# Performance work log

Hardware: AMD Instinct MI355X
Metric: run time of the kernel (lower is better)

The kernel has to match this reference:

```python
import jax, jax.numpy as jnp
import numpy as np


def setup_inputs() -> dict:
    key = jax.random.key(0)
    ks = jax.random.split(key, 5)
    B, S, D, H, E = 2, 2048, 1024, 2816, 8
    x = jax.random.normal(ks[0], (B, S, D), dtype=jnp.float32)
    Wg = jax.random.normal(ks[1], (E, D), dtype=jnp.float32) * 0.02
    W1 = jax.random.normal(ks[2], (E, H, D), dtype=jnp.float32) * 0.02
    W2 = jax.random.normal(ks[3], (E, H, D), dtype=jnp.float32) * 0.02
    W3 = jax.random.normal(ks[4], (E, D, H), dtype=jnp.float32) * 0.02
    return {"x": x, "Wg": Wg, "W1": W1, "W2": W2, "W3": W3}


TOP_K = 2


def reference(x, Wg, W1, W2, W3):
    B, S, D = x.shape
    E = Wg.shape[0]
    xt = x.reshape(B * S, D)  # [T, D]
    # gating: raw logits, NO softmax (matches original module)
    scores = xt @ Wg.T  # [T, E]
    topk_scores, topk_idx = jax.lax.top_k(scores, TOP_K)  # [T, K]
    # dense per-expert SwiGLU FFN over all tokens, combined with sparse weights
    gate = jax.nn.silu(jnp.einsum('td,ehd->teh', xt, W1))  # [T, E, H]
    up = jnp.einsum('td,ehd->teh', xt, W2)                 # [T, E, H]
    y = jnp.einsum('teh,edh->ted', gate * up, W3)           # [T, E, D]
    # combine weights: w[t, e] = sum_k topk_scores[t, k] * (topk_idx[t, k] == e)
    onehot = jax.nn.one_hot(topk_idx, E, dtype=x.dtype)     # [T, K, E]
    w = jnp.einsum('tke,tk->te', onehot, topk_scores)       # [T, E]
    out = jnp.einsum('te,ted->td', w, y)                    # [T, D]
    return out.reshape(B, S, D)
```

## Files before the change

kernel.cpp:

```cpp
#include <hip/hip_runtime.h>
#include <hip/hip_bf16.h>


#define T_TOK 4096
#define DDIM 1024
#define HDIM 2816
#define NEXP 8

typedef __attribute__((ext_vector_type(8))) short short8;
typedef __attribute__((ext_vector_type(4))) short short4v;
typedef __attribute__((ext_vector_type(4))) float floatx4;

__device__ __forceinline__ short f2bf(float f) {
  union { float f; unsigned int u; } v; v.f = f;
  unsigned int u = v.u;
  u += 0x7FFFu + ((u >> 16) & 1u);
  return (short)(u >> 16);
}

__global__ __launch_bounds__(256) void zero_kernel(float4* __restrict__ out4, int* __restrict__ counts) {
  int i = blockIdx.x * 256 + threadIdx.x;
  out4[i] = make_float4(0.f, 0.f, 0.f, 0.f);
  if (blockIdx.x == 0 && threadIdx.x < NEXP) counts[threadIdx.x] = 0;
}

__global__ __launch_bounds__(64) void gating_kernel(const float* __restrict__ x,
    const float* __restrict__ Wg, short* __restrict__ xbf,
    int* __restrict__ counts, int* __restrict__ tlist, float* __restrict__ wlist) {
  int t = blockIdx.x;
  int lane = threadIdx.x;
  const float* xt = x + (size_t)t * DDIM;
  float xr[16];
#pragma unroll
  for (int j = 0; j < 16; ++j) xr[j] = xt[j * 64 + lane];
  short* xbt = xbf + (size_t)t * DDIM;
#pragma unroll
  for (int j = 0; j < 16; ++j) xbt[j * 64 + lane] = f2bf(xr[j]);
  float s[NEXP];
#pragma unroll
  for (int e = 0; e < NEXP; ++e) {
    const float* wge = Wg + e * DDIM;
    float p = 0.f;
#pragma unroll
    for (int j = 0; j < 16; ++j) p += xr[j] * wge[j * 64 + lane];
#pragma unroll
    for (int o = 32; o > 0; o >>= 1) p += __shfl_xor(p, o, 64);
    s[e] = p;
  }
  if (lane == 0) {
    int e1 = 0; float s1 = s[0];
#pragma unroll
    for (int e = 1; e < NEXP; ++e) if (s[e] > s1) { s1 = s[e]; e1 = e; }
    int e2 = -1; float s2 = -1e30f;
#pragma unroll
    for (int e = 0; e < NEXP; ++e) if (e != e1 && s[e] > s2) { s2 = s[e]; e2 = e; }
    int slot = atomicAdd(&counts[e1], 1);
    tlist[e1 * T_TOK + slot] = t; wlist[e1 * T_TOK + slot] = s1;
    slot = atomicAdd(&counts[e2], 1);
    tlist[e2 * T_TOK + slot] = t; wlist[e2 * T_TOK + slot] = s2;
  }
}

__global__ void offsets_kernel(const int* __restrict__ counts, int* __restrict__ offs) {
  if (threadIdx.x == 0 && blockIdx.x == 0) {
    int run = 0;
    for (int e = 0; e < NEXP; ++e) { offs[e] = run; run += counts[e]; }
  }
}

__global__ __launch_bounds__(256) void ffn1_kernel(const short* __restrict__ xbf,
    const float* __restrict__ W1, const float* __restrict__ W2,
    const int* __restrict__ counts, const int* __restrict__ offs,
    const int* __restrict__ tlist, short* __restrict__ hmat) {
  int e = blockIdx.z;
  int cnt = counts[e];
  int m0 = blockIdx.y * 128;
  if (m0 >= cnt) return;
  int n0 = blockIdx.x * 64;
  __shared__ __attribute__((aligned(16))) short As[128 * 40];
  __shared__ __attribute__((aligned(16))) short Bs1[64 * 40];
  __shared__ __attribute__((aligned(16))) short Bs2[64 * 40];
  __shared__ int toks[128];
  int tid = threadIdx.x;
  if (tid < 128) {
    int m = m0 + tid;
    toks[tid] = tlist[e * T_TOK + (m < cnt ? m : cnt - 1)];
  }
  __syncthreads();
  const float* W1e = W1 + (size_t)e * HDIM * DDIM + (size_t)n0 * DDIM;
  const float* W2e = W2 + (size_t)e * HDIM * DDIM + (size_t)n0 * DDIM;
  int lane = tid & 63, wid = tid >> 6;
  int wr = wid >> 1, wc = wid & 1;
  int lrow = lane & 15, lq = lane >> 4;
  floatx4 accg[4][2], accu[4][2];
#pragma unroll
  for (int i = 0; i < 4; ++i)
#pragma unroll
    for (int j = 0; j < 2; ++j) {
      accg[i][j] = (floatx4){0.f, 0.f, 0.f, 0.f};
      accu[i][j] = (floatx4){0.f, 0.f, 0.f, 0.f};
    }
  int ar0 = tid >> 2, ac0 = (tid & 3) * 8;
  int br0 = tid >> 3, bc0 = (tid & 7) * 4;
  int tokA0 = toks[ar0], tokA1 = toks[ar0 + 64];
  const short* xA0 = xbf + (size_t)tokA0 * DDIM + ac0;
  const short* xA1 = xbf + (size_t)tokA1 * DDIM + ac0;
  const float* pB1a = W1e + (size_t)br0 * DDIM + bc0;
  const float* pB1b = W1e + (size_t)(br0 + 32) * DDIM + bc0;
  const float* pB2a = W2e + (size_t)br0 * DDIM + bc0;
  const float* pB2b = W2e + (size_t)(br0 + 32) * DDIM + bc0;

  for (int kk = 0; kk < DDIM; kk += 32) {
    *(short8*)&As[ar0 * 40 + ac0]        = *(const short8*)(xA0 + kk);
    *(short8*)&As[(ar0 + 64) * 40 + ac0] = *(const short8*)(xA1 + kk);
    {
      float4 v1a = *(const float4*)(pB1a + kk);
      float4 v1b = *(const float4*)(pB1b + kk);
      float4 v2a = *(const float4*)(pB2a + kk);
      float4 v2b = *(const float4*)(pB2b + kk);
      *(short4v*)&Bs1[br0 * 40 + bc0]        = (short4v){f2bf(v1a.x), f2bf(v1a.y), f2bf(v1a.z), f2bf(v1a.w)};
      *(short4v*)&Bs1[(br0 + 32) * 40 + bc0] = (short4v){f2bf(v1b.x), f2bf(v1b.y), f2bf(v1b.z), f2bf(v1b.w)};
      *(short4v*)&Bs2[br0 * 40 + bc0]        = (short4v){f2bf(v2a.x), f2bf(v2a.y), f2bf(v2a.z), f2bf(v2a.w)};
      *(short4v*)&Bs2[(br0 + 32) * 40 + bc0] = (short4v){f2bf(v2b.x), f2bf(v2b.y), f2bf(v2b.z), f2bf(v2b.w)};
    }
    __syncthreads();
    short8 a[4], b1[2], b2[2];
#pragma unroll
    for (int mf = 0; mf < 4; ++mf)
      a[mf] = *(short8*)&As[(wr * 64 + mf * 16 + lrow) * 40 + lq * 8];
#pragma unroll
    for (int nf = 0; nf < 2; ++nf) {
      b1[nf] = *(short8*)&Bs1[(wc * 32 + nf * 16 + lrow) * 40 + lq * 8];
      b2[nf] = *(short8*)&Bs2[(wc * 32 + nf * 16 + lrow) * 40 + lq * 8];
    }
#pragma unroll
    for (int mf = 0; mf < 4; ++mf)
#pragma unroll
      for (int nf = 0; nf < 2; ++nf) {
        accg[mf][nf] = __builtin_amdgcn_mfma_f32_16x16x32_bf16(a[mf], b1[nf], accg[mf][nf], 0, 0, 0);
        accu[mf][nf] = __builtin_amdgcn_mfma_f32_16x16x32_bf16(a[mf], b2[nf], accu[mf][nf], 0, 0, 0);
      }
    __syncthreads();
  }
  int base = offs[e];
#pragma unroll
  for (int mf = 0; mf < 4; ++mf)
#pragma unroll
    for (int r = 0; r < 4; ++r) {
      int mloc = wr * 64 + mf * 16 + lq * 4 + r;
      if (m0 + mloc < cnt) {
        size_t row = (size_t)(base + m0 + mloc);
#pragma unroll
        for (int nf = 0; nf < 2; ++nf) {
          float g = accg[mf][nf][r];
          float u = accu[mf][nf][r];
          float h = g / (1.f + __expf(-g)) * u;
          hmat[row * HDIM + n0 + wc * 32 + nf * 16 + lrow] = f2bf(h);
        }
      }
    }
}

__global__ __launch_bounds__(256) void ffn2_kernel(const short* __restrict__ hmat,
    const float* __restrict__ W3,
    const int* __restrict__ counts, const int* __restrict__ offs,
    const int* __restrict__ tlist, const float* __restrict__ wlist,
    float* __restrict__ out) {
  int e = blockIdx.z;
  int cnt = counts[e];
  int m0 = blockIdx.y * 128;
  if (m0 >= cnt) return;
  int n0 = blockIdx.x * 128;
  __shared__ __attribute__((aligned(16))) short As[128 * 40];
  __shared__ __attribute__((aligned(16))) short Bs[128 * 40];
  __shared__ int toks[128];
  __shared__ float wts[128];
  int tid = threadIdx.x;
  if (tid < 128) {
    int m = m0 + tid;
    int mc = m < cnt ? m : cnt - 1;
    toks[tid] = tlist[e * T_TOK + mc];
    wts[tid] = (m < cnt) ? wlist[e * T_TOK + m] : 0.f;
  }
  __syncthreads();
  int base = offs[e];
  const float* W3e = W3 + (size_t)e * DDIM * HDIM + (size_t)n0 * HDIM;
  int lane = tid & 63, wid = tid >> 6;
  int wr = wid >> 1, wc = wid & 1;
  int lrow = lane & 15, lq = lane >> 4;
  floatx4 acc[4][4];
#pragma unroll
  for (int i = 0; i < 4; ++i)
#pragma unroll
    for (int j = 0; j < 4; ++j) acc[i][j] = (floatx4){0.f, 0.f, 0.f, 0.f};
  int ar0 = tid >> 2, ac0 = (tid & 3) * 8;
  int br0 = tid >> 3, bc0 = (tid & 7) * 4;
  int mA0 = m0 + ar0;       mA0 = mA0 < cnt ? mA0 : cnt - 1;
  int mA1 = m0 + ar0 + 64;  mA1 = mA1 < cnt ? mA1 : cnt - 1;
  const short* hA0 = hmat + (size_t)(base + mA0) * HDIM + ac0;
  const short* hA1 = hmat + (size_t)(base + mA1) * HDIM + ac0;

  for (int kk = 0; kk < HDIM; kk += 32) {
    *(short8*)&As[ar0 * 40 + ac0]        = *(const short8*)(hA0 + kk);
    *(short8*)&As[(ar0 + 64) * 40 + ac0] = *(const short8*)(hA1 + kk);
#pragma unroll
    for (int l = 0; l < 4; ++l) {
      int r = br0 + l * 32;
      float4 v = *(const float4*)(W3e + (size_t)r * HDIM + kk + bc0);
      *(short4v*)&Bs[r * 40 + bc0] = (short4v){f2bf(v.x), f2bf(v.y), f2bf(v.z), f2bf(v.w)};
    }
    __syncthreads();
    short8 a[4], b[4];
#pragma unroll
    for (int mf = 0; mf < 4; ++mf)
      a[mf] = *(short8*)&As[(wr * 64 + mf * 16 + lrow) * 40 + lq * 8];
#pragma unroll
    for (int nf = 0; nf < 4; ++nf)
      b[nf] = *(short8*)&Bs[(wc * 64 + nf * 16 + lrow) * 40 + lq * 8];
#pragma unroll
    for (int mf = 0; mf < 4; ++mf)
#pragma unroll
      for (int nf = 0; nf < 4; ++nf)
        acc[mf][nf] = __builtin_amdgcn_mfma_f32_16x16x32_bf16(a[mf], b[nf], acc[mf][nf], 0, 0, 0);
    __syncthreads();
  }
#pragma unroll
  for (int mf = 0; mf < 4; ++mf)
#pragma unroll
    for (int r = 0; r < 4; ++r) {
      int mloc = wr * 64 + mf * 16 + lq * 4 + r;
      if (m0 + mloc < cnt) {
        int t = toks[mloc];
        float w = wts[mloc];
        float* orow = out + (size_t)t * DDIM + n0 + wc * 64 + lrow;
#pragma unroll
        for (int nf = 0; nf < 4; ++nf)
          atomicAdd(orow + nf * 16, w * acc[mf][nf][r]);
      }
    }
}

extern "C" void kernel_launch(void* const* d_in, const int* in_sizes, int n_in,
                              void* d_out, int out_size, void* d_ws, size_t ws_size,
                              hipStream_t stream) {
  const float* x  = (const float*)d_in[0];
  const float* Wg = (const float*)d_in[1];
  const float* W1 = (const float*)d_in[2];
  const float* W2 = (const float*)d_in[3];
  const float* W3 = (const float*)d_in[4];
  float* out = (float*)d_out;
  char* ws = (char*)d_ws;
  int*   counts = (int*)(ws + 0);
  int*   offs   = (int*)(ws + 256);
  int*   tlist  = (int*)(ws + 512);
  float* wlist  = (float*)(ws + 512 + 131072);
  short* xbf    = (short*)(ws + 512 + 2 * 131072);
  short* hmat   = (short*)(ws + 8651264);

  zero_kernel<<<4096, 256, 0, stream>>>((float4*)out, counts);
  gating_kernel<<<4096, 64, 0, stream>>>(x, Wg, xbf, counts, tlist, wlist);
  offsets_kernel<<<1, 64, 0, stream>>>(counts, offs);
  ffn1_kernel<<<dim3(HDIM / 64, T_TOK / 128, NEXP), 256, 0, stream>>>(xbf, W1, W2, counts, offs, tlist, hmat);
  ffn2_kernel<<<dim3(DDIM / 128, T_TOK / 128, NEXP), 256, 0, stream>>>(hmat, W3, counts, offs, tlist, wlist, out);
}
```

Baseline: 653.6 us.

## Pre-convert weights to bf16, use direct global-to-LDS loads, split-K FFN2 with combine

Measured after the change: 622.2 us. -4.8%, faster.

```diff
diff --git a/kernel.cpp b/kernel.cpp
--- a/kernel.cpp
+++ b/kernel.cpp
@@ -1,5 +1,6 @@
 #include <hip/hip_runtime.h>
 #include <hip/hip_bf16.h>
+#include <stdint.h>
 
 
 #define T_TOK 4096
@@ -18,15 +19,39 @@
   return (short)(u >> 16);
 }
 
-__global__ __launch_bounds__(256) void zero_kernel(float4* __restrict__ out4, int* __restrict__ counts) {
-  int i = blockIdx.x * 256 + threadIdx.x;
-  out4[i] = make_float4(0.f, 0.f, 0.f, 0.f);
-  if (blockIdx.x == 0 && threadIdx.x < NEXP) counts[threadIdx.x] = 0;
-}
-
-__global__ __launch_bounds__(64) void gating_kernel(const float* __restrict__ x,
+__device__ __forceinline__ void gl2lds16(const void* g, void* l) {
+  __builtin_amdgcn_global_load_lds(
+      (const __attribute__((address_space(1))) void*)g,
+      (__attribute__((address_space(3))) void*)l, 16, 0, 0);
+}
+
+__global__ void offsets_kernel(const int* __restrict__ counts, int* __restrict__ offs) {
+  if (threadIdx.x == 0 && blockIdx.x == 0) {
+    int run = 0;
+    for (int e = 0; e < NEXP; ++e) { offs[e] = run; run += counts[e]; }
+  }
+}
+
+#define CONV_ELEM4 5767168
+__global__ __launch_bounds__(256) void convert_kernel(
+    const float* __restrict__ W1, const float* __restrict__ W2, const float* __restrict__ W3,
+    short* __restrict__ W1bf, short* __restrict__ W2bf, short* __restrict__ W3bf,
+    int* __restrict__ counts) {
+  if (blockIdx.x == 0 && blockIdx.y == 0 && threadIdx.x < NEXP) counts[threadIdx.x] = 0;
+  int z = blockIdx.y;
+  const float4* src = (const float4*)((z == 0) ? W1 : (z == 1) ? W2 : W3);
+  short4v* dst = (short4v*)((z == 0) ? W1bf : (z == 1) ? W2bf : W3bf);
+  size_t stride = (size_t)gridDim.x * 256;
+  for (size_t i = (size_t)blockIdx.x * 256 + threadIdx.x; i < CONV_ELEM4; i += stride) {
+    float4 v = src[i];
+    dst[i] = (short4v){f2bf(v.x), f2bf(v.y), f2bf(v.z), f2bf(v.w)};
+  }
+}
+
+__global__ __launch_bounds__(64) void gating_fast_kernel(const float* __restrict__ x,
     const float* __restrict__ Wg, short* __restrict__ xbf,
-    int* __restrict__ counts, int* __restrict__ tlist, float* __restrict__ wlist) {
+    int* __restrict__ counts, int* __restrict__ tlist,
+    int* __restrict__ re, int* __restrict__ rs, float* __restrict__ rw) {
   int t = blockIdx.x;
   int lane = threadIdx.x;
   const float* xt = x + (size_t)t * DDIM;
@@ -55,21 +80,16 @@
 #pragma unroll
     for (int e = 0; e < NEXP; ++e) if (e != e1 && s[e] > s2) { s2 = s[e]; e2 = e; }
     int slot = atomicAdd(&counts[e1], 1);
-    tlist[e1 * T_TOK + slot] = t; wlist[e1 * T_TOK + slot] = s1;
+    tlist[e1 * T_TOK + slot] = t;
+    re[2 * t] = e1; rs[2 * t] = slot; rw[2 * t] = s1;
     slot = atomicAdd(&counts[e2], 1);
-    tlist[e2 * T_TOK + slot] = t; wlist[e2 * T_TOK + slot] = s2;
-  }
-}
-
-__global__ void offsets_kernel(const int* __restrict__ counts, int* __restrict__ offs) {
-  if (threadIdx.x == 0 && blockIdx.x == 0) {
-    int run = 0;
-    for (int e = 0; e < NEXP; ++e) { offs[e] = run; run += counts[e]; }
-  }
-}
-
-__global__ __launch_bounds__(256) void ffn1_kernel(const short* __restrict__ xbf,
-    const float* __restrict__ W1, const float* __restrict__ W2,
+    tlist[e2 * T_TOK + slot] = t;
+    re[2 * t + 1] = e2; rs[2 * t + 1] = slot; rw[2 * t + 1] = s2;
+  }
+}
+
+__global__ __launch_bounds__(256) void ffn1_fast_kernel(const short* __restrict__ xbf,
+    const short* __restrict__ W1bf, const short* __restrict__ W2bf,
     const int* __restrict__ counts, const int* __restrict__ offs,
     const int* __restrict__ tlist, short* __restrict__ hmat) {
   int e = blockIdx.z;
@@ -77,9 +97,9 @@
   int m0 = blockIdx.y * 128;
   if (m0 >= cnt) return;
   int n0 = blockIdx.x * 64;
-  __shared__ __attribute__((aligned(16))) short As[128 * 40];
-  __shared__ __attribute__((aligned(16))) short Bs1[64 * 40];
-  __shared__ __attribute__((aligned(16))) short Bs2[64 * 40];
+  __shared__ __attribute__((aligned(16))) short As[128 * 32];
+  __shared__ __attribute__((aligned(16))) short Bs1[64 * 32];
+  __shared__ __attribute__((aligned(16))) short Bs2[64 * 32];
   __shared__ int toks[128];
   int tid = threadIdx.x;
   if (tid < 128) {
@@ -87,11 +107,21 @@
     toks[tid] = tlist[e * T_TOK + (m < cnt ? m : cnt - 1)];
   }
   __syncthreads();
-  const float* W1e = W1 + (size_t)e * HDIM * DDIM + (size_t)n0 * DDIM;
-  const float* W2e = W2 + (size_t)e * HDIM * DDIM + (size_t)n0 * DDIM;
-  int lane = tid & 63, wid = tid >> 6;
-  int wr = wid >> 1, wc = wid & 1;
+  int lane = tid & 63, w = tid >> 6;
+  int wr = w >> 1, wc = w & 1;
   int lrow = lane & 15, lq = lane >> 4;
+  int lr = lane >> 2;
+  int lc = (lane & 3) * 8;
+  const short* pA0 = xbf + (size_t)toks[w * 32 + lr] * DDIM + lc;
+  const short* pA1 = xbf + (size_t)toks[w * 32 + 16 + lr] * DDIM + lc;
+  const short* b1e = W1bf + (size_t)e * HDIM * DDIM;
+  const short* b2e = W2bf + (size_t)e * HDIM * DDIM;
+  const short* pB1 = b1e + (size_t)(n0 + w * 16 + lr) * DDIM + lc;
+  const short* pB2 = b2e + (size_t)(n0 + w * 16 + lr) * DDIM + lc;
+  void* lA0 = (void*)&As[(2 * w) * 512];
+  void* lA1 = (void*)&As[(2 * w + 1) * 512];
+  void* lB1 = (void*)&Bs1[w * 512];
+  void* lB2 = (void*)&Bs2[w * 512];
   floatx4 accg[4][2], accu[4][2];
 #pragma unroll
   for (int i = 0; i < 4; ++i)
@@ -100,38 +130,21 @@
       accg[i][j] = (floatx4){0.f, 0.f, 0.f, 0.f};
       accu[i][j] = (floatx4){0.f, 0.f, 0.f, 0.f};
     }
-  int ar0 = tid >> 2, ac0 = (tid & 3) * 8;
-  int br0 = tid >> 3, bc0 = (tid & 7) * 4;
-  int tokA0 = toks[ar0], tokA1 = toks[ar0 + 64];
-  const short* xA0 = xbf + (size_t)tokA0 * DDIM + ac0;
-  const short* xA1 = xbf + (size_t)tokA1 * DDIM + ac0;
-  const float* pB1a = W1e + (size_t)br0 * DDIM + bc0;
-  const float* pB1b = W1e + (size_t)(br0 + 32) * DDIM + bc0;
-  const float* pB2a = W2e + (size_t)br0 * DDIM + bc0;
-  const float* pB2b = W2e + (size_t)(br0 + 32) * DDIM + bc0;
-
   for (int kk = 0; kk < DDIM; kk += 32) {
-    *(short8*)&As[ar0 * 40 + ac0]        = *(const short8*)(xA0 + kk);
-    *(short8*)&As[(ar0 + 64) * 40 + ac0] = *(const short8*)(xA1 + kk);
-    {
-      float4 v1a = *(const float4*)(pB1a + kk);
-      float4 v1b = *(const float4*)(pB1b + kk);
-      float4 v2a = *(const float4*)(pB2a + kk);
-      float4 v2b = *(const float4*)(pB2b + kk);
-      *(short4v*)&Bs1[br0 * 40 + bc0]        = (short4v){f2bf(v1a.x), f2bf(v1a.y), f2bf(v1a.z), f2bf(v1a.w)};
-      *(short4v*)&Bs1[(br0 + 32) * 40 + bc0] = (short4v){f2bf(v1b.x), f2bf(v1b.y), f2bf(v1b.z), f2bf(v1b.w)};
-      *(short4v*)&Bs2[br0 * 40 + bc0]        = (short4v){f2bf(v2a.x), f2bf(v2a.y), f2bf(v2a.z), f2bf(v2a.w)};
-      *(short4v*)&Bs2[(br0 + 32) * 40 + bc0] = (short4v){f2bf(v2b.x), f2bf(v2b.y), f2bf(v2b.z), f2bf(v2b.w)};
-    }
+    gl2lds16(pA0, lA0);
+    gl2lds16(pA1, lA1);
+    gl2lds16(pB1, lB1);
+    gl2lds16(pB2, lB2);
+    pA0 += 32; pA1 += 32; pB1 += 32; pB2 += 32;
     __syncthreads();
     short8 a[4], b1[2], b2[2];
 #pragma unroll
     for (int mf = 0; mf < 4; ++mf)
-      a[mf] = *(short8*)&As[(wr * 64 + mf * 16 + lrow) * 40 + lq * 8];
+      a[mf] = *(short8*)&As[(wr * 64 + mf * 16 + lrow) * 32 + lq * 8];
 #pragma unroll
     for (int nf = 0; nf < 2; ++nf) {
-      b1[nf] = *(short8*)&Bs1[(wc * 32 + nf * 16 + lrow) * 40 + lq * 8];
-      b2[nf] = *(short8*)&Bs2[(wc * 32 + nf * 16 + lrow) * 40 + lq * 8];
+      b1[nf] = *(short8*)&Bs1[(wc * 32 + nf * 16 + lrow) * 32 + lq * 8];
+      b2[nf] = *(short8*)&Bs2[(wc * 32 + nf * 16 + lrow) * 32 + lq * 8];
     }
 #pragma unroll
     for (int mf = 0; mf < 4; ++mf)
@@ -161,62 +174,59 @@
     }
 }
 
-__global__ __launch_bounds__(256) void ffn2_kernel(const short* __restrict__ hmat,
-    const float* __restrict__ W3,
+#define KSPLIT 2
+#define KHALF (HDIM / KSPLIT)
+__global__ __launch_bounds__(256) void ffn2_fast_kernel(const short* __restrict__ hmat,
+    const short* __restrict__ W3bf,
     const int* __restrict__ counts, const int* __restrict__ offs,
-    const int* __restrict__ tlist, const float* __restrict__ wlist,
-    float* __restrict__ out) {
+    float* __restrict__ ypart0, float* __restrict__ ypart1) {
   int e = blockIdx.z;
   int cnt = counts[e];
   int m0 = blockIdx.y * 128;
   if (m0 >= cnt) return;
-  int n0 = blockIdx.x * 128;
-  __shared__ __attribute__((aligned(16))) short As[128 * 40];
-  __shared__ __attribute__((aligned(16))) short Bs[128 * 40];
-  __shared__ int toks[128];
-  __shared__ float wts[128];
+  int ks = blockIdx.x >> 3;
+  int n0 = (blockIdx.x & 7) * 128;
+  int k0 = ks * KHALF;
+  float* ypart = ks ? ypart1 : ypart0;
+  int base = offs[e];
+  __shared__ __attribute__((aligned(16))) short As[128 * 32];
+  __shared__ __attribute__((aligned(16))) short Bs[128 * 32];
   int tid = threadIdx.x;
-  if (tid < 128) {
-    int m = m0 + tid;
-    int mc = m < cnt ? m : cnt - 1;
-    toks[tid] = tlist[e * T_TOK + mc];
-    wts[tid] = (m < cnt) ? wlist[e * T_TOK + m] : 0.f;
-  }
-  __syncthreads();
-  int base = offs[e];
-  const float* W3e = W3 + (size_t)e * DDIM * HDIM + (size_t)n0 * HDIM;
-  int lane = tid & 63, wid = tid >> 6;
-  int wr = wid >> 1, wc = wid & 1;
+  int lane = tid & 63, w = tid >> 6;
+  int wr = w >> 1, wc = w & 1;
   int lrow = lane & 15, lq = lane >> 4;
+  int lr = lane >> 2;
+  int lc = (lane & 3) * 8;
+  int gA0 = m0 + w * 32 + lr;      gA0 = gA0 < cnt ? gA0 : cnt - 1;
+  int gA1 = m0 + w * 32 + 16 + lr; gA1 = gA1 < cnt ? gA1 : cnt - 1;
+  const short* pA0 = hmat + (size_t)(base + gA0) * HDIM + k0 + lc;
+  const short* pA1 = hmat + (size_t)(base + gA1) * HDIM + k0 + lc;
+  const short* W3e = W3bf + (size_t)e * DDIM * HDIM;
+  const short* pB0 = W3e + (size_t)(n0 + w * 32 + lr) * HDIM + k0 + lc;
+  const short* pB1 = W3e + (size_t)(n0 + w * 32 + 16 + lr) * HDIM + k0 + lc;
+  void* lA0 = (void*)&As[(2 * w) * 512];
+  void* lA1 = (void*)&As[(2 * w + 1) * 512];
+  void* lB0 = (void*)&Bs[(2 * w) * 512];
+  void* lB1 = (void*)&Bs[(2 * w + 1) * 512];
   floatx4 acc[4][4];
 #pragma unroll
   for (int i = 0; i < 4; ++i)
 #pragma unroll
     for (int j = 0; j < 4; ++j) acc[i][j] = (floatx4){0.f, 0.f, 0.f, 0.f};
-  int ar0 = tid >> 2, ac0 = (tid & 3) * 8;
-  int br0 = tid >> 3, bc0 = (tid & 7) * 4;
-  int mA0 = m0 + ar0;       mA0 = mA0 < cnt ? mA0 : cnt - 1;
-  int mA1 = m0 + ar0 + 64;  mA1 = mA1 < cnt ? mA1 : cnt - 1;
-  const short* hA0 = hmat + (size_t)(base + mA0) * HDIM + ac0;
-  const short* hA1 = hmat + (size_t)(base + mA1) * HDIM + ac0;
-
-  for (int kk = 0; kk < HDIM; kk += 32) {
-    *(short8*)&As[ar0 * 40 + ac0]        = *(const short8*)(hA0 + kk);
-    *(short8*)&As[(ar0 + 64) * 40 + ac0] = *(const short8*)(hA1 + kk);
-#pragma unroll
-    for (int l = 0; l < 4; ++l) {
-      int r = br0 + l * 32;
-      float4 v = *(const float4*)(W3e + (size_t)r * HDIM + kk + bc0);
-      *(short4v*)&Bs[r * 40 + bc0] = (short4v){f2bf(v.x), f2bf(v.y), f2bf(v.z), f2bf(v.w)};
-    }
+  for (int kk = 0; kk < KHALF; kk += 32) {
+    gl2lds16(pA0, lA0);
+    gl2lds16(pA1, lA1);
+    gl2lds16(pB0, lB0);
+    gl2lds16(pB1, lB1);
+    pA0 += 32; pA1 += 32; pB0 += 32; pB1 += 32;
     __syncthreads();
     short8 a[4], b[4];
 #pragma unroll
     for (int mf = 0; mf < 4; ++mf)
-      a[mf] = *(short8*)&As[(wr * 64 + mf * 16 + lrow) * 40 + lq * 8];
+      a[mf] = *(short8*)&As[(wr * 64 + mf * 16 + lrow) * 32 + lq * 8];
 #pragma unroll
     for (int nf = 0; nf < 4; ++nf)
-      b[nf] = *(short8*)&Bs[(wc * 64 + nf * 16 + lrow) * 40 + lq * 8];
+      b[nf] = *(short8*)&Bs[(wc * 64 + nf * 16 + lrow) * 32 + lq * 8];
 #pragma unroll
     for (int mf = 0; mf < 4; ++mf)
 #pragma unroll
@@ -230,14 +240,30 @@
     for (int r = 0; r < 4; ++r) {
       int mloc = wr * 64 + mf * 16 + lq * 4 + r;
       if (m0 + mloc < cnt) {
-        int t = toks[mloc];
-        float w = wts[mloc];
-        float* orow = out + (size_t)t * DDIM + n0 + wc * 64 + lrow;
+        float* orow = ypart + (size_t)(base + m0 + mloc) * DDIM + n0 + wc * 64 + lrow;
 #pragma unroll
         for (int nf = 0; nf < 4; ++nf)
-          atomicAdd(orow + nf * 16, w * acc[mf][nf][r]);
+          orow[nf * 16] = acc[mf][nf][r];
       }
     }
+}
+
+__global__ __launch_bounds__(256) void combine_kernel(const float4* __restrict__ y0,
+    const float4* __restrict__ y1,
+    const int* __restrict__ offs, const int* __restrict__ re, const int* __restrict__ rs,
+    const float* __restrict__ rw, float4* __restrict__ out4) {
+  int t = blockIdx.x;
+  int i = threadIdx.x;
+  size_t r0 = (size_t)(offs[re[2 * t]] + rs[2 * t]) * 256 + i;
+  size_t r1 = (size_t)(offs[re[2 * t + 1]] + rs[2 * t + 1]) * 256 + i;
+  float w0 = rw[2 * t], w1 = rw[2 * t + 1];
+  float4 a0 = y0[r0], a1 = y1[r0];
+  float4 b0 = y0[r1], b1 = y1[r1];
+  out4[(size_t)t * 256 + i] = make_float4(
+      w0 * (a0.x + a1.x) + w1 * (b0.x + b1.x),
+      w0 * (a0.y + a1.y) + w1 * (b0.y + b1.y),
+      w0 * (a0.z + a1.z) + w1 * (b0.z + b1.z),
+      w0 * (a0.w + a1.w) + w1 * (b0.w + b1.w));
 }
 
 extern "C" void kernel_launch(void* const* d_in, const int* in_sizes, int n_in,
@@ -250,16 +276,28 @@
   const float* W3 = (const float*)d_in[4];
   float* out = (float*)d_out;
   char* ws = (char*)d_ws;
+
   int*   counts = (int*)(ws + 0);
   int*   offs   = (int*)(ws + 256);
   int*   tlist  = (int*)(ws + 512);
-  float* wlist  = (float*)(ws + 512 + 131072);
-  short* xbf    = (short*)(ws + 512 + 2 * 131072);
-  short* hmat   = (short*)(ws + 8651264);
-
-  zero_kernel<<<4096, 256, 0, stream>>>((float4*)out, counts);
-  gating_kernel<<<4096, 64, 0, stream>>>(x, Wg, xbf, counts, tlist, wlist);
+  int*   re     = (int*)(ws + 131584);
+  int*   rs     = (int*)(ws + 164352);
+  float* rw     = (float*)(ws + 197120);
+  short* xbf    = (short*)(ws + 229888);
+  short* hmat   = (short*)(ws + 8618496);
+  short* W3bf   = (short*)(ws + 54755840);
+  short* W1bf   = (short*)(ws + 100893184);
+  short* W2bf   = (short*)(ws + 147030528);
+  float* ypart0 = (float*)(ws + 100893184);
+  float* ypart1 = (float*)(ws + 147030528);
+
+  convert_kernel<<<dim3(4096, 3), 256, 0, stream>>>(W1, W2, W3, W1bf, W2bf, W3bf, counts);
+  gating_fast_kernel<<<T_TOK, 64, 0, stream>>>(x, Wg, xbf, counts, tlist, re, rs, rw);
   offsets_kernel<<<1, 64, 0, stream>>>(counts, offs);
-  ffn1_kernel<<<dim3(HDIM / 64, T_TOK / 128, NEXP), 256, 0, stream>>>(xbf, W1, W2, counts, offs, tlist, hmat);
-  ffn2_kernel<<<dim3(DDIM / 128, T_TOK / 128, NEXP), 256, 0, stream>>>(hmat, W3, counts, offs, tlist, wlist, out);
-}
+  ffn1_fast_kernel<<<dim3(HDIM / 64, T_TOK / 128, NEXP), 256, 0, stream>>>(
+      xbf, W1bf, W2bf, counts, offs, tlist, hmat);
+  ffn2_fast_kernel<<<dim3((DDIM / 128) * KSPLIT, T_TOK / 128, NEXP), 256, 0, stream>>>(
+      hmat, W3bf, counts, offs, ypart0, ypart1);
+  combine_kernel<<<T_TOK, 256, 0, stream>>>((const float4*)ypart0, (const float4*)ypart1,
+                                            offs, re, rs, rw, (float4*)out);
+}
```
